# Performance work log

Measured on AMD Instinct MI355X. Metric: run time of the kernel, lower is better.

The kernel has to match this reference:

```python
import jax, jax.numpy as jnp
import numpy as np

N_EMB = 1024
N_HEAD = 16
HEAD_SIZE = N_EMB // N_HEAD  # 64
B, T = 4, 4096


def setup_inputs() -> dict:
    key = jax.random.key(0)
    kx, kq, kk, kv = jax.random.split(key, 4)
    x = jax.random.normal(kx, (B, T, N_EMB), dtype=jnp.float32)
    # torch nn.Linear(in=N_EMB, out=HEAD_SIZE, bias=False) weight: [out, in]
    s = 1.0 / np.sqrt(N_EMB)
    Wq = jax.random.uniform(kq, (HEAD_SIZE, N_EMB), jnp.float32, -s, s)
    Wk = jax.random.uniform(kk, (HEAD_SIZE, N_EMB), jnp.float32, -s, s)
    Wv = jax.random.uniform(kv, (HEAD_SIZE, N_EMB), jnp.float32, -s, s)
    return {"x": x, "Wq": Wq, "Wk": Wk, "Wv": Wv}


def reference(x, Wq, Wk, Wv):
    # q,k,v: [B,T,H]
    q = jnp.einsum('btc,hc->bth', x, Wq)
    k = jnp.einsum('btc,hc->bth', x, Wk)
    v = jnp.einsum('btc,hc->bth', x, Wv)
    scale = HEAD_SIZE ** (-0.5)
    att = jnp.einsum('bth,bsh->bts', q, k) * scale  # [B,T,T]
    Tn = x.shape[1]
    causal = jnp.tril(jnp.ones((Tn, Tn), dtype=bool))
    att = jnp.where(causal, att, -jnp.inf)
    att = jax.nn.softmax(att, axis=-1)
    # dropout p=0.0 -> identity
    out = jnp.einsum('bts,bsh->bth', att, v)  # [B,T,H]
    return out
```

## Files before the change

kernel.cpp:

```cpp
#include <hip/hip_runtime.h>


typedef __attribute__((ext_vector_type(8))) short v8s;
typedef __attribute__((ext_vector_type(4))) float v4f;

static __device__ __forceinline__ unsigned short f2bf(float x) {
  unsigned int u = __builtin_bit_cast(unsigned int, x);
  u += 0x7fffu + ((u >> 16) & 1u);
  return (unsigned short)(u >> 16);
}

static __device__ __forceinline__ void dma16(const void* src, void* dst) {
  __builtin_amdgcn_global_load_lds(
      (const __attribute__((address_space(1))) void*)src,
      (__attribute__((address_space(3))) void*)dst, 16, 0, 0);
}

__global__ __launch_bounds__(256) void pack_w(const float* __restrict__ Wq,
                                              const float* __restrict__ Wk,
                                              const float* __restrict__ Wv,
                                              unsigned short* __restrict__ WF) {
  int idx = (blockIdx.x * 256 + threadIdx.x) * 4;
  int row = idx >> 10;
  int k   = idx & 1023;
  const float* src;
  float scale;
  if (row < 64)       { src = Wq + row * 1024 + k;         scale = 0.125f; }
  else if (row < 128) { src = Wk + (row - 64) * 1024 + k;  scale = 1.0f;   }
  else                { src = Wv + (row - 128) * 1024 + k; scale = 1.0f;   }
  float4 f = *(const float4*)src;
  ushort4 o;
  o.x = f2bf(f.x * scale); o.y = f2bf(f.y * scale);
  o.z = f2bf(f.z * scale); o.w = f2bf(f.w * scale);
  size_t off = ((size_t)(k >> 5) * 12 + (row >> 4)) * 512 +
               (((k >> 3) & 3) * 16 + (row & 15)) * 8 + (k & 7);
  *(ushort4*)(WF + off) = o;
}

__global__ __launch_bounds__(128) void qkv(const float* __restrict__ x,
                                           const unsigned short* __restrict__ WF,
                                           unsigned short* __restrict__ Qg,
                                           unsigned short* __restrict__ KF,
                                           unsigned short* __restrict__ VF) {
  __shared__ alignas(16) char xs[2][8192];
  __shared__ alignas(16) char ws[2][24576];
  const int tid   = threadIdx.x;
  const int lane  = tid & 63;
  const int wv    = tid >> 6;
  const int quad  = lane >> 4;
  const int colid = lane & 15;
  const int row0  = blockIdx.x * 32;

  const char* xB = (const char*)x;
  const char* WB = (const char*)WF;

  v4f acc[12];
#pragma unroll
  for (int i = 0; i < 12; i++) acc[i] = (v4f){0.f, 0.f, 0.f, 0.f};

  auto stage = [&](int kt, int slot) {
#pragma unroll
    for (int i = 0; i < 4; i++) {
      int c   = wv * 4 + i;
      int cwv = c >> 2, s = (c >> 1) & 1, h = c & 1;
      const char* src = xB + (size_t)(row0 + cwv * 16 + colid) * 4096 +
                        kt * 256 + s * 128 + quad * 32 + h * 16;
      dma16(src, &xs[slot][c * 1024]);
    }
#pragma unroll
    for (int i = 0; i < 12; i++) {
      int id = wv * 12 + i;
      int s = id / 12, nt = id % 12;
      const char* src = WB + ((size_t)(kt * 2 + s) * 12 + nt) * 1024 + lane * 16;
      dma16(src, &ws[slot][id * 1024]);
    }
  };

  stage(0, 0);

  for (int kt = 0; kt < 16; kt++) {
    const int slot = kt & 1;
    __syncthreads();
    if (kt < 15) stage(kt + 1, slot ^ 1);
#pragma unroll
    for (int s = 0; s < 2; s++) {
      float4 f0 = *(const float4*)(&xs[slot][(wv * 4 + s * 2 + 0) * 1024 + lane * 16]);
      float4 f1 = *(const float4*)(&xs[slot][(wv * 4 + s * 2 + 1) * 1024 + lane * 16]);
      v8s a;
      a[0] = (short)f2bf(f0.x); a[1] = (short)f2bf(f0.y);
      a[2] = (short)f2bf(f0.z); a[3] = (short)f2bf(f0.w);
      a[4] = (short)f2bf(f1.x); a[5] = (short)f2bf(f1.y);
      a[6] = (short)f2bf(f1.z); a[7] = (short)f2bf(f1.w);
#pragma unroll
      for (int nt = 0; nt < 12; nt++) {
        v8s b = *(const v8s*)(&ws[slot][(s * 12 + nt) * 1024 + lane * 16]);
        acc[nt] = __builtin_amdgcn_mfma_f32_16x16x32_bf16(a, b, acc[nt], 0, 0, 0);
      }
    }
  }

  const int trow_base = row0 + wv * 16 + quad * 4;
#pragma unroll
  for (int nt = 0; nt < 12; nt++) {
    if (nt < 4) {
#pragma unroll
      for (int r = 0; r < 4; r++)
        Qg[(size_t)(trow_base + r) * 64 + nt * 16 + colid] = f2bf(acc[nt][r]);
    } else if (nt < 8) {
      int half = (nt - 4) >> 1;
      int q_f  = ((nt - 4) * 2 + (colid >> 3)) & 3;
      int j    = colid & 7;
#pragma unroll
      for (int r = 0; r < 4; r++) {
        int t  = trow_base + r;
        int b  = t >> 12, tl = t & 4095;
        int si = tl >> 6, sl = tl & 63;
        KF[((size_t)(b * 64 + si) * 8 + (sl >> 4) * 2 + half) * 512 +
           (q_f * 16 + (sl & 15)) * 8 + j] = f2bf(acc[nt][r]);
      }
    } else {
#pragma unroll
      for (int r = 0; r < 4; r++) {
        int t  = trow_base + r;
        int b  = t >> 12, tl = t & 4095;
        int si = tl >> 6;
        int half = (tl >> 5) & 1, q_f = (tl >> 3) & 3, j = tl & 7;
        VF[((size_t)(b * 64 + si) * 8 + (nt - 8) * 2 + half) * 512 +
           (q_f * 16 + colid) * 8 + j] = f2bf(acc[nt][r]);
      }
    }
  }
}

__global__ __launch_bounds__(256, 2) void flash(const unsigned short* __restrict__ Qg,
                                                const unsigned short* __restrict__ KF,
                                                const unsigned short* __restrict__ VF,
                                                float* __restrict__ out) {
  __shared__ alignas(16) char smem[4 * 32 * 68 * 4 + 4 * 32 * 4];
  unsigned short* pl = (unsigned short*)smem;
  float* redf = (float*)smem;
  float* lred = (float*)(smem + 4 * 32 * 68 * 4);

  const int tid   = threadIdx.x;
  const int lane  = tid & 63;
  const int wv    = tid >> 6;
  const int quad  = lane >> 4;
  const int colid = lane & 15;
  const int qt32  = 127 - (int)(blockIdx.x >> 2);
  const int b     = blockIdx.x & 3;
  const int bT    = b * 4096;
  const int row00 = qt32 * 32;
  const int qimax = (row00 + 31) >> 6;

  v8s qf[2][2];
#pragma unroll
  for (int mt = 0; mt < 2; mt++) {
    const unsigned short* qrow =
        Qg + (size_t)(bT + row00 + mt * 16 + colid) * 64 + quad * 8;
    qf[mt][0] = *(const v8s*)(qrow);
    qf[mt][1] = *(const v8s*)(qrow + 32);
  }

  v8s ones;
#pragma unroll
  for (int j = 0; j < 8; j++) ones[j] = (short)0x3F80;

  v4f o[2][4];
#pragma unroll
  for (int mt = 0; mt < 2; mt++)
#pragma unroll
    for (int i = 0; i < 4; i++) o[mt][i] = (v4f){0.f, 0.f, 0.f, 0.f};
  v4f lac[2];
  lac[0] = (v4f){0.f, 0.f, 0.f, 0.f};
  lac[1] = (v4f){0.f, 0.f, 0.f, 0.f};

  const unsigned short* kb0 = KF + (size_t)b * 64 * 4096 + lane * 8;
  const unsigned short* vb0 = VF + (size_t)b * 64 * 4096 + lane * 8;

  for (int si = wv; si <= qimax; si += 4) {
    const unsigned short* ktile = kb0 + (size_t)si * 4096;
    const unsigned short* vtile = vb0 + (size_t)si * 4096;
    v8s ck[8], cv[8];
#pragma unroll
    for (int c = 0; c < 8; c++) ck[c] = *(const v8s*)(ktile + (size_t)c * 512);
#pragma unroll
    for (int c = 0; c < 8; c++) cv[c] = *(const v8s*)(vtile + (size_t)c * 512);

#pragma unroll
    for (int mt = 0; mt < 2; mt++) {
      v4f s[4];
#pragma unroll
      for (int i = 0; i < 4; i++) s[i] = (v4f){0.f, 0.f, 0.f, 0.f};
#pragma unroll
      for (int nt = 0; nt < 4; nt++) {
        s[nt] = __builtin_amdgcn_mfma_f32_16x16x32_bf16(qf[mt][0], ck[2 * nt], s[nt], 0, 0, 0);
        s[nt] = __builtin_amdgcn_mfma_f32_16x16x32_bf16(qf[mt][1], ck[2 * nt + 1], s[nt], 0, 0, 0);
      }

      if (si == qimax) {
        int rowb = row00 + mt * 16 + quad * 4;
        int colb = si * 64;
#pragma unroll
        for (int nt = 0; nt < 4; nt++)
#pragma unroll
          for (int r = 0; r < 4; r++)
            if (colb + nt * 16 + colid > rowb + r) s[nt][r] = -1e30f;
      }

      unsigned short* pw = pl + (wv * 2 + mt) * (16 * 72);
#pragma unroll
      for (int nt = 0; nt < 4; nt++)
#pragma unroll
        for (int r = 0; r < 4; r++)
          pw[(quad * 4 + r) * 72 + nt * 16 + colid] = f2bf(__expf(s[nt][r]));
    }

#pragma unroll
    for (int mt = 0; mt < 2; mt++) {
      unsigned short* pw = pl + (wv * 2 + mt) * (16 * 72);
#pragma unroll
      for (int ks = 0; ks < 64; ks += 32) {
        v8s af = *(const v8s*)(&pw[colid * 72 + ks + quad * 8]);
        lac[mt] = __builtin_amdgcn_mfma_f32_16x16x32_bf16(af, ones, lac[mt], 0, 0, 0);
#pragma unroll
        for (int nt = 0; nt < 4; nt++)
          o[mt][nt] = __builtin_amdgcn_mfma_f32_16x16x32_bf16(
              af, cv[2 * nt + (ks >> 5)], o[mt][nt], 0, 0, 0);
      }
    }
  }

  __syncthreads();
#pragma unroll
  for (int mt = 0; mt < 2; mt++) {
#pragma unroll
    for (int nt = 0; nt < 4; nt++)
#pragma unroll
      for (int r = 0; r < 4; r++)
        redf[(wv * 32 + mt * 16 + quad * 4 + r) * 68 + nt * 16 + colid] = o[mt][nt][r];
    if (colid == 0) {
#pragma unroll
      for (int r = 0; r < 4; r++)
        lred[wv * 32 + mt * 16 + quad * 4 + r] = lac[mt][r];
    }
  }
  __syncthreads();

  {
    int col = tid & 63;
    int r0  = tid >> 6;
#pragma unroll
    for (int rr = 0; rr < 8; rr++) {
      int row = r0 * 8 + rr;
      float sum = 0.f, lsum = 0.f;
#pragma unroll
      for (int w = 0; w < 4; w++) {
        sum  += redf[(w * 32 + row) * 68 + col];
        lsum += lred[w * 32 + row];
      }
      out[(size_t)(bT + row00 + row) * 64 + col] = sum / lsum;
    }
  }
}

extern "C" void kernel_launch(void* const* d_in, const int* in_sizes, int n_in,
                              void* d_out, int out_size, void* d_ws, size_t ws_size,
                              hipStream_t stream) {
  const float* x  = (const float*)d_in[0];
  const float* Wq = (const float*)d_in[1];
  const float* Wk = (const float*)d_in[2];
  const float* Wv = (const float*)d_in[3];
  float* out = (float*)d_out;

  unsigned short* WF = (unsigned short*)d_ws;
  unsigned short* Qg = WF + 192 * 1024;
  unsigned short* KF = Qg + 16384 * 64;
  unsigned short* VF = KF + 16384 * 64;

  hipLaunchKernelGGL(pack_w, dim3(192), dim3(256), 0, stream, Wq, Wk, Wv, WF);
  hipLaunchKernelGGL(qkv, dim3(512), dim3(128), 0, stream, x, WF, Qg, KF, VF);
  hipLaunchKernelGGL(flash, dim3(512), dim3(256), 0, stream, Qg, KF, VF, out);
}
```

Baseline: 143.0 us.

## Restructure QKV projection to 64-row tiles with per-wave output column split

The QKV projection kernel now processes 64 rows per block with 4 waves. Each wave computes 3 of the 12 output column tiles across all 64 rows, instead of each wave computing all 12 columns for 16 rows. Weights are no longer staged through LDS; each wave loads its B fragments directly from global memory, which is likely L2-resident. This halves the grid, enlarges the x staging buffer, and removes weight LDS traffic. In exchange, each wave re-converts x to bf16 four times per k-step, and weight reads now go to global memory and can add latency.

Result: faster. 136.9 us (-4.3%).

```diff
diff --git a/kernel.cpp b/kernel.cpp
--- a/kernel.cpp
+++ b/kernel.cpp
@@ -37,22 +37,21 @@
   *(ushort4*)(WF + off) = o;
 }
 
-__global__ __launch_bounds__(128) void qkv(const float* __restrict__ x,
+__global__ __launch_bounds__(256) void qkv(const float* __restrict__ x,
                                            const unsigned short* __restrict__ WF,
                                            unsigned short* __restrict__ Qg,
                                            unsigned short* __restrict__ KF,
                                            unsigned short* __restrict__ VF) {
-  __shared__ alignas(16) char xs[2][8192];
-  __shared__ alignas(16) char ws[2][24576];
+  __shared__ alignas(16) char xs[2][32768];
   const int tid   = threadIdx.x;
   const int lane  = tid & 63;
   const int wv    = tid >> 6;
   const int quad  = lane >> 4;
   const int colid = lane & 15;
-  const int row0  = blockIdx.x * 32;
+  const int row0  = blockIdx.x * 64;
 
   const char* xB = (const char*)x;
-  const char* WB = (const char*)WF;
+  const unsigned short* wf = WF + lane * 8;
 
   v4f acc[12];
 #pragma unroll
@@ -60,73 +59,78 @@
 
   auto stage = [&](int kt, int slot) {
 #pragma unroll
-    for (int i = 0; i < 4; i++) {
-      int c   = wv * 4 + i;
-      int cwv = c >> 2, s = (c >> 1) & 1, h = c & 1;
-      const char* src = xB + (size_t)(row0 + cwv * 16 + colid) * 4096 +
-                        kt * 256 + s * 128 + quad * 32 + h * 16;
-      dma16(src, &xs[slot][c * 1024]);
-    }
-#pragma unroll
-    for (int i = 0; i < 12; i++) {
-      int id = wv * 12 + i;
-      int s = id / 12, nt = id % 12;
-      const char* src = WB + ((size_t)(kt * 2 + s) * 12 + nt) * 1024 + lane * 16;
-      dma16(src, &ws[slot][id * 1024]);
+    for (int i = 0; i < 8; i++) {
+      int id = wv * 8 + i;
+      int s = (id >> 1) & 3, h = id & 1;
+      const char* src = xB + (size_t)(row0 + wv * 16 + colid) * 4096 +
+                        kt * 512 + s * 128 + quad * 32 + h * 16;
+      dma16(src, &xs[slot][id * 1024]);
     }
   };
 
   stage(0, 0);
 
-  for (int kt = 0; kt < 16; kt++) {
+  for (int kt = 0; kt < 8; kt++) {
     const int slot = kt & 1;
     __syncthreads();
-    if (kt < 15) stage(kt + 1, slot ^ 1);
-#pragma unroll
-    for (int s = 0; s < 2; s++) {
-      float4 f0 = *(const float4*)(&xs[slot][(wv * 4 + s * 2 + 0) * 1024 + lane * 16]);
-      float4 f1 = *(const float4*)(&xs[slot][(wv * 4 + s * 2 + 1) * 1024 + lane * 16]);
-      v8s a;
-      a[0] = (short)f2bf(f0.x); a[1] = (short)f2bf(f0.y);
-      a[2] = (short)f2bf(f0.z); a[3] = (short)f2bf(f0.w);
-      a[4] = (short)f2bf(f1.x); a[5] = (short)f2bf(f1.y);
-      a[6] = (short)f2bf(f1.z); a[7] = (short)f2bf(f1.w);
-#pragma unroll
-      for (int nt = 0; nt < 12; nt++) {
-        v8s b = *(const v8s*)(&ws[slot][(s * 12 + nt) * 1024 + lane * 16]);
-        acc[nt] = __builtin_amdgcn_mfma_f32_16x16x32_bf16(a, b, acc[nt], 0, 0, 0);
-      }
-    }
-  }
-
-  const int trow_base = row0 + wv * 16 + quad * 4;
-#pragma unroll
-  for (int nt = 0; nt < 12; nt++) {
-    if (nt < 4) {
-#pragma unroll
-      for (int r = 0; r < 4; r++)
-        Qg[(size_t)(trow_base + r) * 64 + nt * 16 + colid] = f2bf(acc[nt][r]);
-    } else if (nt < 8) {
-      int half = (nt - 4) >> 1;
-      int q_f  = ((nt - 4) * 2 + (colid >> 3)) & 3;
-      int j    = colid & 7;
-#pragma unroll
-      for (int r = 0; r < 4; r++) {
-        int t  = trow_base + r;
-        int b  = t >> 12, tl = t & 4095;
-        int si = tl >> 6, sl = tl & 63;
-        KF[((size_t)(b * 64 + si) * 8 + (sl >> 4) * 2 + half) * 512 +
-           (q_f * 16 + (sl & 15)) * 8 + j] = f2bf(acc[nt][r]);
-      }
-    } else {
-#pragma unroll
-      for (int r = 0; r < 4; r++) {
-        int t  = trow_base + r;
-        int b  = t >> 12, tl = t & 4095;
-        int si = tl >> 6;
-        int half = (tl >> 5) & 1, q_f = (tl >> 3) & 3, j = tl & 7;
-        VF[((size_t)(b * 64 + si) * 8 + (nt - 8) * 2 + half) * 512 +
-           (q_f * 16 + colid) * 8 + j] = f2bf(acc[nt][r]);
+    if (kt < 7) stage(kt + 1, slot ^ 1);
+#pragma unroll
+    for (int s = 0; s < 4; s++) {
+      const int g = kt * 4 + s;
+      v8s bw[3];
+#pragma unroll
+      for (int ntl = 0; ntl < 3; ntl++)
+        bw[ntl] = *(const v8s*)(wf + ((size_t)g * 12 + wv * 3 + ntl) * 512);
+#pragma unroll
+      for (int mg = 0; mg < 4; mg++) {
+        float4 f0 = *(const float4*)(&xs[slot][(mg * 8 + s * 2 + 0) * 1024 + lane * 16]);
+        float4 f1 = *(const float4*)(&xs[slot][(mg * 8 + s * 2 + 1) * 1024 + lane * 16]);
+        v8s a;
+        a[0] = (short)f2bf(f0.x); a[1] = (short)f2bf(f0.y);
+        a[2] = (short)f2bf(f0.z); a[3] = (short)f2bf(f0.w);
+        a[4] = (short)f2bf(f1.x); a[5] = (short)f2bf(f1.y);
+        a[6] = (short)f2bf(f1.z); a[7] = (short)f2bf(f1.w);
+#pragma unroll
+        for (int ntl = 0; ntl < 3; ntl++)
+          acc[mg * 3 + ntl] =
+              __builtin_amdgcn_mfma_f32_16x16x32_bf16(a, bw[ntl], acc[mg * 3 + ntl], 0, 0, 0);
+      }
+    }
+  }
+
+#pragma unroll
+  for (int ntl = 0; ntl < 3; ntl++) {
+    const int nt = wv * 3 + ntl;
+#pragma unroll
+    for (int mg = 0; mg < 4; mg++) {
+      const int trow_base = row0 + mg * 16 + quad * 4;
+      if (nt < 4) {
+#pragma unroll
+        for (int r = 0; r < 4; r++)
+          Qg[(size_t)(trow_base + r) * 64 + nt * 16 + colid] =
+              f2bf(acc[mg * 3 + ntl][r]);
+      } else if (nt < 8) {
+        int half = (nt - 4) >> 1;
+        int q_f  = ((nt - 4) * 2 + (colid >> 3)) & 3;
+        int j    = colid & 7;
+#pragma unroll
+        for (int r = 0; r < 4; r++) {
+          int t  = trow_base + r;
+          int b  = t >> 12, tl = t & 4095;
+          int si = tl >> 6, sl = tl & 63;
+          KF[((size_t)(b * 64 + si) * 8 + (sl >> 4) * 2 + half) * 512 +
+             (q_f * 16 + (sl & 15)) * 8 + j] = f2bf(acc[mg * 3 + ntl][r]);
+        }
+      } else {
+#pragma unroll
+        for (int r = 0; r < 4; r++) {
+          int t  = trow_base + r;
+          int b  = t >> 12, tl = t & 4095;
+          int si = tl >> 6;
+          int half = (tl >> 5) & 1, q_f = (tl >> 3) & 3, j = tl & 7;
+          VF[((size_t)(b * 64 + si) * 8 + (nt - 8) * 2 + half) * 512 +
+             (q_f * 16 + colid) * 8 + j] = f2bf(acc[mg * 3 + ntl][r]);
+        }
       }
     }
   }
@@ -278,6 +282,6 @@
   unsigned short* VF = KF + 16384 * 64;
 
   hipLaunchKernelGGL(pack_w, dim3(192), dim3(256), 0, stream, Wq, Wk, Wv, WF);
-  hipLaunchKernelGGL(qkv, dim3(512), dim3(128), 0, stream, x, WF, Qg, KF, VF);
+  hipLaunchKernelGGL(qkv, dim3(256), dim3(256), 0, stream, x, WF, Qg, KF, VF);
   hipLaunchKernelGGL(flash, dim3(512), dim3(256), 0, stream, Qg, KF, VF, out);
 }
```
